# Performance work log

Hardware: AMD Instinct MI355X
Metric: run time of the kernel (lower is better)

## Reference

```python
import jax, jax.numpy as jnp
import numpy as np
from functools import partial

B, S, I, H, L = 32, 512, 512, 512, 2  # batch, seq, input, hidden, layers (bidirectional)


def _uniform(key, shape, k):
    return jax.random.uniform(key, shape, jnp.float32, -k, k)


def setup_inputs() -> dict:
    key = jax.random.key(0)
    keys = jax.random.split(key, 1 + 16)
    inp = {"x": jax.random.normal(keys[0], (B, S, I), jnp.float32)}
    k = 1.0 / H
    ki = 1
    for l in range(L):
        in_sz = I if l == 0 else 2 * H
        for d in ("f", "b"):
            inp[f"w_ih_{l}{d}"] = _uniform(keys[ki], (4 * H, in_sz), k); ki += 1
            inp[f"w_hh_{l}{d}"] = _uniform(keys[ki], (4 * H, H), k); ki += 1
            inp[f"b_ih_{l}{d}"] = _uniform(keys[ki], (4 * H,), k); ki += 1
            inp[f"b_hh_{l}{d}"] = _uniform(keys[ki], (4 * H,), k); ki += 1
    return inp


def _lstm_dir(x_sbi, w_ih, w_hh, b_ih, b_hh, reverse):
    # x_sbi: [S,B,in]. Precompute input projection for all timesteps (one big GEMM).
    xp = jnp.einsum('sbi,gi->sbg', x_sbi, w_ih) + b_ih + b_hh  # [S,B,4H]
    h0 = jnp.zeros((x_sbi.shape[1], H), x_sbi.dtype)
    c0 = jnp.zeros_like(h0)

    def step(carry, xg):
        h, c = carry
        gates = xg + h @ w_hh.T
        i, f, g, o = jnp.split(gates, 4, axis=-1)  # pytorch order i,f,g,o
        i = jax.nn.sigmoid(i); f = jax.nn.sigmoid(f)
        g = jnp.tanh(g); o = jax.nn.sigmoid(o)
        c_new = f * c + i * g
        h_new = o * jnp.tanh(c_new)
        return (h_new, c_new), h_new

    (hT, cT), hs = jax.lax.scan(step, (h0, c0), xp, reverse=reverse)
    return hs, hT, cT  # hs in original time order [S,B,H]


def _forward(x, params):
    seq = jnp.transpose(x, (1, 0, 2))  # [S,B,I]
    final_h, final_c = [], []
    for l in range(L):
        hf, hTf, cTf = _lstm_dir(seq, *params[(l, 'f')], reverse=False)
        hb, hTb, cTb = _lstm_dir(seq, *params[(l, 'b')], reverse=True)
        seq = jnp.concatenate([hf, hb], axis=-1)  # [S,B,2H]
        final_h += [hTf, hTb]; final_c += [cTf, cTb]
    out = jnp.transpose(seq, (1, 0, 2))  # [B,S,2H]
    return out, (jnp.stack(final_h, 0), jnp.stack(final_c, 0))


def reference(x,
              w_ih_0f, w_hh_0f, b_ih_0f, b_hh_0f,
              w_ih_0b, w_hh_0b, b_ih_0b, b_hh_0b,
              w_ih_1f, w_hh_1f, b_ih_1f, b_hh_1f,
              w_ih_1b, w_hh_1b, b_ih_1b, b_hh_1b):
    params = {
        (0, 'f'): (w_ih_0f, w_hh_0f, b_ih_0f, b_hh_0f),
        (0, 'b'): (w_ih_0b, w_hh_0b, b_ih_0b, b_hh_0b),
        (1, 'f'): (w_ih_1f, w_hh_1f, b_ih_1f, b_hh_1f),
        (1, 'b'): (w_ih_1b, w_hh_1b, b_ih_1b, b_hh_1b),
    }
    return _forward(x, params)
```

## Files before the change

### kernel.cpp

```cpp
#include <hip/hip_runtime.h>

#define BB 32
#define SS 512
#define II 512
#define HH 512
#define GG 2048

typedef unsigned short u16;
typedef unsigned int   u32;
typedef unsigned long long u64;

typedef __attribute__((ext_vector_type(8))) short bf16x8;
typedef __attribute__((ext_vector_type(4))) float f32x4;

__device__ __forceinline__ float b2f(u16 h) {
    return __uint_as_float(((u32)h) << 16);
}
__device__ __forceinline__ u16 f2b(float f) {
    u32 u = __float_as_uint(f);
    u32 r = (u + 0x7FFFu + ((u >> 16) & 1u)) >> 16;
    return (u16)r;
}

#ifndef __has_builtin
#define __has_builtin(x) 0
#endif
#if __has_builtin(__builtin_amdgcn_global_load_lds)
#define HAVE_GLL 1
#else
#define HAVE_GLL 0
#endif

typedef __attribute__((address_space(1))) void as1_void;
typedef __attribute__((address_space(3))) void as3_void;

__device__ __forceinline__ void gload16(const void* g, void* l, int lane) {
#if HAVE_GLL
    __builtin_amdgcn_global_load_lds((as1_void*)g, (as3_void*)l, 16, 0, 0);
#else
    *(bf16x8*)((char*)l + lane * 16) = *(const bf16x8*)g;
#endif
}

__global__ void k_convert_x(const float* __restrict__ x, u16* __restrict__ xbf) {
    const int n4 = BB * SS * II / 4;
    for (int e4 = blockIdx.x * blockDim.x + threadIdx.x; e4 < n4;
         e4 += gridDim.x * blockDim.x) {
        int e = e4 * 4;
        int s = e >> 14;
        int b = (e >> 9) & 31;
        int i = e & 511;
        float4 v = *(const float4*)(x + (size_t)b * (SS * II) + (size_t)s * II + i);
        ushort4 o;
        o.x = f2b(v.x); o.y = f2b(v.y); o.z = f2b(v.z); o.w = f2b(v.w);
        *(ushort4*)(xbf + (size_t)s * (BB * II) + (size_t)b * II + i) = o;
    }
}

__global__ void k_cast(const float* __restrict__ src, u16* __restrict__ dst, int n4) {
    for (int e4 = blockIdx.x * blockDim.x + threadIdx.x; e4 < n4;
         e4 += gridDim.x * blockDim.x) {
        float4 v = *(const float4*)(src + (size_t)e4 * 4);
        ushort4 o;
        o.x = f2b(v.x); o.y = f2b(v.y); o.z = f2b(v.z); o.w = f2b(v.w);
        *(ushort4*)(dst + (size_t)e4 * 4) = o;
    }
}

#define BKP 64

__launch_bounds__(256)
__global__ void k_proj(const u16* __restrict__ A,
                       const u16* __restrict__ Wf_, const u16* __restrict__ Wb_,
                       const float* __restrict__ bihf, const float* __restrict__ bhhf,
                       const float* __restrict__ bihb, const float* __restrict__ bhhb,
                       u16* __restrict__ xpf, u16* __restrict__ xpb,
                       int K) {
    const int dir = blockIdx.z;
    const u16* Wm = dir ? Wb_ : Wf_;
    const float* bih = dir ? bihb : bihf;
    const float* bhh = dir ? bhhb : bhhf;
    u16* xp = dir ? xpb : xpf;

    __shared__ __align__(16) u16 As[128 * BKP];
    __shared__ __align__(16) u16 Bs[128 * BKP];

    const int t    = threadIdx.x;
    const int lane = t & 63;
    const int w    = t >> 6;
    const int wm   = w >> 1, wn = w & 1;
    const int m0   = blockIdx.x * 128;
    const int n0   = blockIdx.y * 128;

    f32x4 acc[4][4] = {};

    for (int kt = 0; kt < K; kt += BKP) {
        #pragma unroll
        for (int i = 0; i < 4; ++i) {
            int c   = (w * 4 + i) * 64 + lane;
            int row = c >> 3;
            int lc  = (c & 7) ^ (row & 7);
            int gk  = kt + lc * 8;
            gload16(A  + (size_t)(m0 + row) * K + gk, (char*)As + (w * 4 + i) * 1024, lane);
            gload16(Wm + (size_t)(n0 + row) * K + gk, (char*)Bs + (w * 4 + i) * 1024, lane);
        }
        __syncthreads();

        #pragma unroll
        for (int ks = 0; ks < 2; ++ks) {
            const int kc = ks * 4 + (lane >> 4);
            bf16x8 af[4], bfr[4];
            #pragma unroll
            for (int mi = 0; mi < 4; ++mi) {
                int row = wm * 64 + mi * 16 + (lane & 15);
                af[mi] = *(const bf16x8*)&As[row * BKP + ((kc ^ (row & 7)) << 3)];
            }
            #pragma unroll
            for (int ni = 0; ni < 4; ++ni) {
                int row = wn * 64 + ni * 16 + (lane & 15);
                bfr[ni] = *(const bf16x8*)&Bs[row * BKP + ((kc ^ (row & 7)) << 3)];
            }
            #pragma unroll
            for (int mi = 0; mi < 4; ++mi)
                #pragma unroll
                for (int ni = 0; ni < 4; ++ni)
                    acc[mi][ni] = __builtin_amdgcn_mfma_f32_16x16x32_bf16(
                        af[mi], bfr[ni], acc[mi][ni], 0, 0, 0);
        }
        __syncthreads();
    }

    #pragma unroll
    for (int ni = 0; ni < 4; ++ni) {
        int n = n0 + wn * 64 + ni * 16 + (lane & 15);
        float bias = bih[n] + bhh[n];
        #pragma unroll
        for (int mi = 0; mi < 4; ++mi) {
            #pragma unroll
            for (int r = 0; r < 4; ++r) {
                int m = m0 + wm * 64 + mi * 16 + (lane >> 4) * 4 + r;
                xp[(size_t)m * GG + n] = f2b(acc[mi][ni][r] + bias);
            }
        }
    }
}

__launch_bounds__(256)
__global__ void k_rec(const u16* __restrict__ xpf, const u16* __restrict__ xpb,
                      const float* __restrict__ whf, const float* __restrict__ whb,
                      u16* __restrict__ hbuf,
                      u32* __restrict__ flags,
                      u16* __restrict__ hs0,
                      float* __restrict__ out,
                      float* __restrict__ fin,
                      int layer) {
    const int bid  = blockIdx.x;
    const int dir  = bid >> 5;
    const int wg   = bid & 31;
    const int j0   = wg * 16;
    const u16*  xp = dir ? xpb : xpf;
    const float* W = dir ? whb : whf;
    u32* myflags   = flags + dir * 1024;

    const int t    = threadIdx.x;
    const int lane = t & 63;
    const int g    = t >> 6;

    __shared__ __align__(16) u16 Wfr[64 * 64 * 8];
    __shared__ __align__(16) u16 hl[32 * 512];
    __shared__ float xq[32 * 65];
    __shared__ float gates[4 * 32 * 16];

    for (int it = 0; it < 16; ++it) {
        int task = it * 256 + t;
        int l    = task & 63;
        int blk  = task >> 6;
        int gg   = blk >> 4;
        int kt   = blk & 15;
        const float* src = W + (size_t)(gg * 512 + j0 + (l & 15)) * 512
                             + kt * 32 + (l >> 4) * 8;
        float4 v0 = *(const float4*)src;
        float4 v1 = *(const float4*)(src + 4);
        union { bf16x8 v; u16 a[8]; } u;
        u.a[0] = f2b(v0.x); u.a[1] = f2b(v0.y); u.a[2] = f2b(v0.z); u.a[3] = f2b(v0.w);
        u.a[4] = f2b(v1.x); u.a[5] = f2b(v1.y); u.a[6] = f2b(v1.z); u.a[7] = f2b(v1.w);
        *(bf16x8*)&Wfr[task * 8] = u.v;
    }
    __syncthreads();

    float creg[4] = {0.f, 0.f, 0.f, 0.f};
    const int eb = t & 31;
    const int ej = t >> 5;

    for (int s = 0; s < SS; ++s) {
        const int sa = dir ? (SS - 1 - s) : s;
        const u16* hprev = hbuf + ((size_t)((s & 1) * 2 + dir)) * (32 * 512);
        u16*       hnext = hbuf + ((size_t)(((s & 1) ^ 1) * 2 + dir)) * (32 * 512);

        if (t < 128) {
            int b = t & 31, gq = t >> 5;
            const u16* xsrc = xp + (size_t)(sa * 32 + b) * GG + gq * 512 + j0;
            bf16x8 v0 = *(const bf16x8*)xsrc;
            bf16x8 v1 = *(const bf16x8*)(xsrc + 8);
            #pragma unroll
            for (int i = 0; i < 8; ++i) {
                xq[b * 65 + gq * 16 + i]     = b2f((u16)v0[i]);
                xq[b * 65 + gq * 16 + 8 + i] = b2f((u16)v1[i]);
            }
        }

        if (s > 0 && t < 64) {
            const u32 tgt = (u32)s;
            for (;;) {
                u32 v = tgt;
                if (lane < 32 && lane != wg)
                    v = __hip_atomic_load(myflags + lane * 32, __ATOMIC_RELAXED,
                                          __HIP_MEMORY_SCOPE_AGENT);
                if (__all(v >= tgt)) break;
            }
        }
        __syncthreads();

        {
            int r = t >> 3, seg = t & 7;
            const u64* hp = (const u64*)(hprev + r * 512) + seg * 16;
            u64 v[16];
            #pragma unroll
            for (int i = 0; i < 16; ++i)
                v[i] = __hip_atomic_load(hp + i, __ATOMIC_RELAXED,
                                         __HIP_MEMORY_SCOPE_AGENT);
            u16* lbase = hl + r * 512;
            #pragma unroll
            for (int i2 = 0; i2 < 8; ++i2) {
                int c  = seg * 8 + i2;
                int pc = c ^ (r & 7);
                union { u64 q[2]; bf16x8 v8; } uu;
                uu.q[0] = v[2 * i2]; uu.q[1] = v[2 * i2 + 1];
                *(bf16x8*)(lbase + pc * 8) = uu.v8;
            }
        }
        __syncthreads();

        {
            f32x4 acc0 = {0.f, 0.f, 0.f, 0.f}, acc1 = {0.f, 0.f, 0.f, 0.f};
            const int b0 = lane & 15, q = lane >> 4;
            #pragma unroll
            for (int kt = 0; kt < 16; ++kt) {
                int pc = ((kt << 2) + q) ^ (b0 & 7);
                bf16x8 a0 = *(const bf16x8*)&hl[b0 * 512 + pc * 8];
                bf16x8 a1 = *(const bf16x8*)&hl[(b0 + 16) * 512 + pc * 8];
                bf16x8 Bv = *(const bf16x8*)&Wfr[((g * 16 + kt) * 64 + lane) * 8];
                acc0 = __builtin_amdgcn_mfma_f32_16x16x32_bf16(a0, Bv, acc0, 0, 0, 0);
                acc1 = __builtin_amdgcn_mfma_f32_16x16x32_bf16(a1, Bv, acc1, 0, 0, 0);
            }
            #pragma unroll
            for (int r = 0; r < 4; ++r) {
                gates[g * 512 + (q * 4 + r) * 16 + b0]      = acc0[r];
                gates[g * 512 + (16 + q * 4 + r) * 16 + b0] = acc1[r];
            }
        }
        __syncthreads();

        if (t < 128) {
            float hv[4], cv[4];
            #pragma unroll
            for (int k = 0; k < 4; ++k) {
                int jj = ej * 4 + k;
                float gi = xq[eb * 65 +      jj] + gates[0 * 512 + eb * 16 + jj];
                float gf = xq[eb * 65 + 16 + jj] + gates[1 * 512 + eb * 16 + jj];
                float gg = xq[eb * 65 + 32 + jj] + gates[2 * 512 + eb * 16 + jj];
                float go = xq[eb * 65 + 48 + jj] + gates[3 * 512 + eb * 16 + jj];
                float ig = 1.f / (1.f + __expf(-gi));
                float fg = 1.f / (1.f + __expf(-gf));
                float gt = tanhf(gg);
                float og = 1.f / (1.f + __expf(-go));
                float c  = fg * creg[k] + ig * gt;
                float h  = og * tanhf(c);
                creg[k] = c; cv[k] = c; hv[k] = h;
            }
            union { u64 q; u16 a[4]; } ho;
            #pragma unroll
            for (int k = 0; k < 4; ++k) ho.a[k] = f2b(hv[k]);
            __hip_atomic_store((u64*)(hnext + eb * 512 + j0 + ej * 4), ho.q,
                               __ATOMIC_RELAXED, __HIP_MEMORY_SCOPE_AGENT);
            if (layer == 0) {
                *(u64*)(hs0 + (size_t)sa * (BB * 1024) + (size_t)eb * 1024
                        + dir * 512 + j0 + ej * 4) = ho.q;
            } else {
                float4 ov = make_float4(hv[0], hv[1], hv[2], hv[3]);
                *(float4*)(out + (size_t)eb * (SS * 1024) + (size_t)sa * 1024
                           + dir * 512 + j0 + ej * 4) = ov;
            }
            if (s == SS - 1) {
                int sl = layer * 2 + dir;
                *(float4*)(fin + (size_t)sl * (32 * 512) + eb * 512 + j0 + ej * 4) =
                    make_float4(hv[0], hv[1], hv[2], hv[3]);
                *(float4*)(fin + 65536 + (size_t)sl * (32 * 512) + eb * 512 + j0 + ej * 4) =
                    make_float4(cv[0], cv[1], cv[2], cv[3]);
            }
        }

        asm volatile("s_waitcnt vmcnt(0)" ::: "memory");
        __syncthreads();
        if (t == 0)
            __hip_atomic_store(myflags + wg * 32, (u32)(s + 1), __ATOMIC_RELAXED,
                               __HIP_MEMORY_SCOPE_AGENT);
    }
}

#define OFF_XBF   ((size_t)0)
#define OFF_HS0   ((size_t)16777216)
#define OFF_XPF   ((size_t)50331648)
#define OFF_XPB   ((size_t)117440512)
#define OFF_WIH0F ((size_t)184549376)
#define OFF_WIH0B ((size_t)186646528)
#define OFF_WIH1F ((size_t)188743680)
#define OFF_WIH1B ((size_t)192937984)
#define OFF_H     ((size_t)197132288)
#define OFF_FLAGS ((size_t)197263360)

extern "C" void kernel_launch(void* const* d_in, const int* in_sizes, int n_in,
                              void* d_out, int out_size, void* d_ws, size_t ws_size,
                              hipStream_t stream) {
    const float* x      = (const float*)d_in[0];
    const float* wih0f  = (const float*)d_in[1];
    const float* whh0f  = (const float*)d_in[2];
    const float* bih0f  = (const float*)d_in[3];
    const float* bhh0f  = (const float*)d_in[4];
    const float* wih0b  = (const float*)d_in[5];
    const float* whh0b  = (const float*)d_in[6];
    const float* bih0b  = (const float*)d_in[7];
    const float* bhh0b  = (const float*)d_in[8];
    const float* wih1f  = (const float*)d_in[9];
    const float* whh1f  = (const float*)d_in[10];
    const float* bih1f  = (const float*)d_in[11];
    const float* bhh1f  = (const float*)d_in[12];
    const float* wih1b  = (const float*)d_in[13];
    const float* whh1b  = (const float*)d_in[14];
    const float* bih1b  = (const float*)d_in[15];
    const float* bhh1b  = (const float*)d_in[16];

    float* out = (float*)d_out;
    char* ws = (char*)d_ws;

    u16* xbf    = (u16*)(ws + OFF_XBF);
    u16* hs0    = (u16*)(ws + OFF_HS0);
    u16* xpf    = (u16*)(ws + OFF_XPF);
    u16* xpb    = (u16*)(ws + OFF_XPB);
    u16* bwih0f = (u16*)(ws + OFF_WIH0F);
    u16* bwih0b = (u16*)(ws + OFF_WIH0B);
    u16* bwih1f = (u16*)(ws + OFF_WIH1F);
    u16* bwih1b = (u16*)(ws + OFF_WIH1B);
    u16* hbuf   = (u16*)(ws + OFF_H);
    u32* flags  = (u32*)(ws + OFF_FLAGS);
    float* fin  = out + 16777216;

    k_convert_x<<<1024, 256, 0, stream>>>(x, xbf);
    k_cast<<<512, 256, 0, stream>>>(wih0f, bwih0f, 2048 * 512 / 4);
    k_cast<<<512, 256, 0, stream>>>(wih0b, bwih0b, 2048 * 512 / 4);
    k_cast<<<512, 256, 0, stream>>>(wih1f, bwih1f, 2048 * 1024 / 4);
    k_cast<<<512, 256, 0, stream>>>(wih1b, bwih1b, 2048 * 1024 / 4);

    hipMemsetAsync(ws + OFF_H, 0, 131072, stream);
    hipMemsetAsync(ws + OFF_FLAGS, 0, 8192, stream);
    k_proj<<<dim3(128, 16, 2), 256, 0, stream>>>(
        xbf, bwih0f, bwih0b, bih0f, bhh0f, bih0b, bhh0b, xpf, xpb, 512);
    k_rec<<<64, 256, 0, stream>>>(xpf, xpb, whh0f, whh0b, hbuf, flags,
                                  hs0, nullptr, fin, 0);

    hipMemsetAsync(ws + OFF_H, 0, 131072, stream);
    hipMemsetAsync(ws + OFF_FLAGS, 0, 8192, stream);
    k_proj<<<dim3(128, 16, 2), 256, 0, stream>>>(
        hs0, bwih1f, bwih1b, bih1f, bhh1f, bih1b, bhh1b, xpf, xpb, 1024);
    k_rec<<<64, 256, 0, stream>>>(xpf, xpb, whh1f, whh1b, hbuf, flags,
                                  nullptr, out, fin, 1);
}
```

Measured before the change: 6.075 ms.

## Embed step tags into hidden-state words to replace flag-based inter-block sync

Replaces the per-workgroup flag array and drain/barrier/flag-store protocol with a hidden-state buffer where each bf16 value is packed alongside a layer/step tag in a 32-bit word. Consumers spin directly on the data until all tags match the expected step, which removes the vmcnt drain, an extra barrier and the separate flag round-trip on every timestep. This doubles the bytes exchanged per step and adds polling over 32 loads per thread, and it drops one memset per layer by using tags that include the layer. The elementwise thread mapping and gates padding also change to reduce LDS bank conflicts.

```diff
diff --git a/kernel.cpp b/kernel.cpp
--- a/kernel.cpp
+++ b/kernel.cpp
@@ -148,8 +148,7 @@
 __launch_bounds__(256)
 __global__ void k_rec(const u16* __restrict__ xpf, const u16* __restrict__ xpb,
                       const float* __restrict__ whf, const float* __restrict__ whb,
-                      u16* __restrict__ hbuf,
-                      u32* __restrict__ flags,
+                      u64* __restrict__ Hd,
                       u16* __restrict__ hs0,
                       float* __restrict__ out,
                       float* __restrict__ fin,
@@ -160,7 +159,6 @@
     const int j0   = wg * 16;
     const u16*  xp = dir ? xpb : xpf;
     const float* W = dir ? whb : whf;
-    u32* myflags   = flags + dir * 1024;
 
     const int t    = threadIdx.x;
     const int lane = t & 63;
@@ -169,7 +167,7 @@
     __shared__ __align__(16) u16 Wfr[64 * 64 * 8];
     __shared__ __align__(16) u16 hl[32 * 512];
     __shared__ float xq[32 * 65];
-    __shared__ float gates[4 * 32 * 16];
+    __shared__ float gates[4 * 32 * 18];
 
     for (int it = 0; it < 16; ++it) {
         int task = it * 256 + t;
@@ -189,13 +187,14 @@
     __syncthreads();
 
     float creg[4] = {0.f, 0.f, 0.f, 0.f};
-    const int eb = t & 31;
-    const int ej = t >> 5;
+    const int eb = t >> 2;
+    const int ej = t & 3;
+
+    const int sc_c   = t >> 2;
+    const int sc_sub = (t & 3) * 4;
 
     for (int s = 0; s < SS; ++s) {
         const int sa = dir ? (SS - 1 - s) : s;
-        const u16* hprev = hbuf + ((size_t)((s & 1) * 2 + dir)) * (32 * 512);
-        u16*       hnext = hbuf + ((size_t)(((s & 1) ^ 1) * 2 + dir)) * (32 * 512);
 
         if (t < 128) {
             int b = t & 31, gq = t >> 5;
@@ -209,34 +208,41 @@
             }
         }
 
-        if (s > 0 && t < 64) {
-            const u32 tgt = (u32)s;
+        if (s > 0) {
+            const u64* Hrd = Hd + ((size_t)((s & 1) * 2 + dir)) * (32 * 256);
+            const u32 tgt = (u32)((layer << 10) | s);
             for (;;) {
-                u32 v = tgt;
-                if (lane < 32 && lane != wg)
-                    v = __hip_atomic_load(myflags + lane * 32, __ATOMIC_RELAXED,
+                u64 w = __hip_atomic_load(Hrd + t, __ATOMIC_RELAXED,
                                           __HIP_MEMORY_SCOPE_AGENT);
-                if (__all(v >= tgt)) break;
-            }
-        }
-        __syncthreads();
-
-        {
-            int r = t >> 3, seg = t & 7;
-            const u64* hp = (const u64*)(hprev + r * 512) + seg * 16;
-            u64 v[16];
-            #pragma unroll
-            for (int i = 0; i < 16; ++i)
-                v[i] = __hip_atomic_load(hp + i, __ATOMIC_RELAXED,
-                                         __HIP_MEMORY_SCOPE_AGENT);
-            u16* lbase = hl + r * 512;
-            #pragma unroll
-            for (int i2 = 0; i2 < 8; ++i2) {
-                int c  = seg * 8 + i2;
-                int pc = c ^ (r & 7);
-                union { u64 q[2]; bf16x8 v8; } uu;
-                uu.q[0] = v[2 * i2]; uu.q[1] = v[2 * i2 + 1];
-                *(bf16x8*)(lbase + pc * 8) = uu.v8;
+                bool f = (((u32)w & 0xffffu) == tgt) &&
+                         ((((u32)(w >> 32)) & 0xffffu) == tgt);
+                if (__all(f)) break;
+            }
+            u64 v[32];
+            for (;;) {
+                #pragma unroll
+                for (int i = 0; i < 32; ++i)
+                    v[i] = __hip_atomic_load(Hrd + i * 256 + t, __ATOMIC_RELAXED,
+                                             __HIP_MEMORY_SCOPE_AGENT);
+                bool ok = true;
+                #pragma unroll
+                for (int i = 0; i < 32; ++i) {
+                    ok = ok && (((u32)v[i] & 0xffffu) == tgt);
+                    ok = ok && ((((u32)(v[i] >> 32)) & 0xffffu) == tgt);
+                }
+                if (__all(ok)) break;
+            }
+            #pragma unroll
+            for (int i = 0; i < 32; ++i) {
+                u32 two = ((u32)(v[i] >> 16) & 0xffffu) | (((u32)(v[i] >> 48)) << 16);
+                int off = i * 1024 + ((sc_c ^ (i & 7)) << 4) + sc_sub;
+                *(u32*)((char*)hl + off) = two;
+            }
+        } else {
+            #pragma unroll
+            for (int i = 0; i < 32; ++i) {
+                int off = i * 1024 + ((sc_c ^ (i & 7)) << 4) + sc_sub;
+                *(u32*)((char*)hl + off) = 0u;
             }
         }
         __syncthreads();
@@ -255,56 +261,61 @@
             }
             #pragma unroll
             for (int r = 0; r < 4; ++r) {
-                gates[g * 512 + (q * 4 + r) * 16 + b0]      = acc0[r];
-                gates[g * 512 + (16 + q * 4 + r) * 16 + b0] = acc1[r];
+                gates[g * 576 + (q * 4 + r) * 18 + b0]      = acc0[r];
+                gates[g * 576 + (16 + q * 4 + r) * 18 + b0] = acc1[r];
             }
         }
         __syncthreads();
 
         if (t < 128) {
-            float hv[4], cv[4];
+            float hv4[4], cv4[4];
             #pragma unroll
             for (int k = 0; k < 4; ++k) {
                 int jj = ej * 4 + k;
-                float gi = xq[eb * 65 +      jj] + gates[0 * 512 + eb * 16 + jj];
-                float gf = xq[eb * 65 + 16 + jj] + gates[1 * 512 + eb * 16 + jj];
-                float gg = xq[eb * 65 + 32 + jj] + gates[2 * 512 + eb * 16 + jj];
-                float go = xq[eb * 65 + 48 + jj] + gates[3 * 512 + eb * 16 + jj];
+                float gi = xq[eb * 65 +      jj] + gates[0 * 576 + eb * 18 + jj];
+                float gf = xq[eb * 65 + 16 + jj] + gates[1 * 576 + eb * 18 + jj];
+                float gg = xq[eb * 65 + 32 + jj] + gates[2 * 576 + eb * 18 + jj];
+                float go = xq[eb * 65 + 48 + jj] + gates[3 * 576 + eb * 18 + jj];
                 float ig = 1.f / (1.f + __expf(-gi));
                 float fg = 1.f / (1.f + __expf(-gf));
                 float gt = tanhf(gg);
                 float og = 1.f / (1.f + __expf(-go));
                 float c  = fg * creg[k] + ig * gt;
                 float h  = og * tanhf(c);
-                creg[k] = c; cv[k] = c; hv[k] = h;
-            }
+                creg[k] = c; cv4[k] = c; hv4[k] = h;
+            }
+            u64* Hwr = Hd + ((size_t)(((s + 1) & 1) * 2 + dir)) * (32 * 256);
+            const u32 pst = (u32)((layer << 10) | (s + 1));
+            u32 w0 = ((u32)f2b(hv4[0]) << 16) | pst;
+            u32 w1 = ((u32)f2b(hv4[1]) << 16) | pst;
+            u32 w2 = ((u32)f2b(hv4[2]) << 16) | pst;
+            u32 w3 = ((u32)f2b(hv4[3]) << 16) | pst;
+            u64* dst = Hwr + eb * 256 + ((j0 + ej * 4) >> 1);
+            __hip_atomic_store(dst,     (u64)w0 | ((u64)w1 << 32),
+                               __ATOMIC_RELAXED, __HIP_MEMORY_SCOPE_AGENT);
+            __hip_atomic_store(dst + 1, (u64)w2 | ((u64)w3 << 32),
+                               __ATOMIC_RELAXED, __HIP_MEMORY_SCOPE_AGENT);
+
             union { u64 q; u16 a[4]; } ho;
             #pragma unroll
-            for (int k = 0; k < 4; ++k) ho.a[k] = f2b(hv[k]);
-            __hip_atomic_store((u64*)(hnext + eb * 512 + j0 + ej * 4), ho.q,
-                               __ATOMIC_RELAXED, __HIP_MEMORY_SCOPE_AGENT);
+            for (int k = 0; k < 4; ++k) ho.a[k] = f2b(hv4[k]);
             if (layer == 0) {
                 *(u64*)(hs0 + (size_t)sa * (BB * 1024) + (size_t)eb * 1024
                         + dir * 512 + j0 + ej * 4) = ho.q;
             } else {
-                float4 ov = make_float4(hv[0], hv[1], hv[2], hv[3]);
                 *(float4*)(out + (size_t)eb * (SS * 1024) + (size_t)sa * 1024
-                           + dir * 512 + j0 + ej * 4) = ov;
+                           + dir * 512 + j0 + ej * 4) =
+                    make_float4(hv4[0], hv4[1], hv4[2], hv4[3]);
             }
             if (s == SS - 1) {
                 int sl = layer * 2 + dir;
                 *(float4*)(fin + (size_t)sl * (32 * 512) + eb * 512 + j0 + ej * 4) =
-                    make_float4(hv[0], hv[1], hv[2], hv[3]);
+                    make_float4(hv4[0], hv4[1], hv4[2], hv4[3]);
                 *(float4*)(fin + 65536 + (size_t)sl * (32 * 512) + eb * 512 + j0 + ej * 4) =
-                    make_float4(cv[0], cv[1], cv[2], cv[3]);
-            }
-        }
-
-        asm volatile("s_waitcnt vmcnt(0)" ::: "memory");
-        __syncthreads();
-        if (t == 0)
-            __hip_atomic_store(myflags + wg * 32, (u32)(s + 1), __ATOMIC_RELAXED,
-                               __HIP_MEMORY_SCOPE_AGENT);
+                    make_float4(cv4[0], cv4[1], cv4[2], cv4[3]);
+            }
+        }
+        __syncthreads();
     }
 }
 
@@ -316,8 +327,7 @@
 #define OFF_WIH0B ((size_t)186646528)
 #define OFF_WIH1F ((size_t)188743680)
 #define OFF_WIH1B ((size_t)192937984)
-#define OFF_H     ((size_t)197132288)
-#define OFF_FLAGS ((size_t)197263360)
+#define OFF_HST   ((size_t)197132288)
 
 extern "C" void kernel_launch(void* const* d_in, const int* in_sizes, int n_in,
                               void* d_out, int out_size, void* d_ws, size_t ws_size,
@@ -351,8 +361,7 @@
     u16* bwih0b = (u16*)(ws + OFF_WIH0B);
     u16* bwih1f = (u16*)(ws + OFF_WIH1F);
     u16* bwih1b = (u16*)(ws + OFF_WIH1B);
-    u16* hbuf   = (u16*)(ws + OFF_H);
-    u32* flags  = (u32*)(ws + OFF_FLAGS);
+    u64* Hd     = (u64*)(ws + OFF_HST);
     float* fin  = out + 16777216;
 
     k_convert_x<<<1024, 256, 0, stream>>>(x, xbf);
@@ -361,17 +370,15 @@
     k_cast<<<512, 256, 0, stream>>>(wih1f, bwih1f, 2048 * 1024 / 4);
     k_cast<<<512, 256, 0, stream>>>(wih1b, bwih1b, 2048 * 1024 / 4);
 
-    hipMemsetAsync(ws + OFF_H, 0, 131072, stream);
-    hipMemsetAsync(ws + OFF_FLAGS, 0, 8192, stream);
+    hipMemsetAsync(ws + OFF_HST, 0, 262144, stream);
+
     k_proj<<<dim3(128, 16, 2), 256, 0, stream>>>(
         xbf, bwih0f, bwih0b, bih0f, bhh0f, bih0b, bhh0b, xpf, xpb, 512);
-    k_rec<<<64, 256, 0, stream>>>(xpf, xpb, whh0f, whh0b, hbuf, flags,
+    k_rec<<<64, 256, 0, stream>>>(xpf, xpb, whh0f, whh0b, Hd,
                                   hs0, nullptr, fin, 0);
 
-    hipMemsetAsync(ws + OFF_H, 0, 131072, stream);
-    hipMemsetAsync(ws + OFF_FLAGS, 0, 8192, stream);
     k_proj<<<dim3(128, 16, 2), 256, 0, stream>>>(
         hs0, bwih1f, bwih1b, bih1f, bhh1f, bih1b, bhh1b, xpf, xpb, 1024);
-    k_rec<<<64, 256, 0, stream>>>(xpf, xpb, whh1f, whh1b, hbuf, flags,
+    k_rec<<<64, 256, 0, stream>>>(xpf, xpb, whh1f, whh1b, Hd,
                                   nullptr, out, fin, 1);
 }
```

Measured after the change: 5.243 ms. 1.16x faster.
